# Performance work log

Hardware: AMD Instinct MI355X
Metric: run time of the kernel (lower is better)

Reference implementation:

```python
import jax, jax.numpy as jnp
import numpy as np

HEADS = 8


def setup_inputs() -> dict:
    key = jax.random.key(0)
    ks = jax.random.split(key, 5)
    B, C, H, W = 2, 256, 48, 48
    s = 0.02
    return {
        "ct": jax.random.normal(ks[0], (B, C, H, W), jnp.float32),
        "us": jax.random.normal(ks[1], (B, C, H, W), jnp.float32),
        "w_qkv_ct": jax.random.normal(ks[2], (3 * C, C), jnp.float32) * s,
        "w_qkv_us": jax.random.normal(ks[3], (3 * C, C), jnp.float32) * s,
        "w_proj": jax.random.normal(ks[4], (C, 2 * C), jnp.float32) * s,
        "b_proj": jnp.zeros((C,), jnp.float32),
    }


def _heads_view(x, B, H, W):
    # [B, C, H, W] -> [B, heads, HW, dh]
    C = x.shape[1]
    return x.reshape(B, HEADS, C // HEADS, H * W).transpose(0, 1, 3, 2)


def _cross_attn(q, k, v, scale):
    # q,k,v: [B, heads, HW, dh]
    attn = jax.nn.softmax(jnp.einsum("bhnd,bhmd->bhnm", q, k) * scale, axis=-1)
    return jnp.einsum("bhnm,bhmd->bhnd", attn, v)


def reference(ct, us, w_qkv_ct, w_qkv_us, w_proj, b_proj):
    B, C, H, W = ct.shape
    dh = C // HEADS
    scale = dh ** (-0.5)

    # 1x1 convs as channel GEMMs
    qkv1 = jnp.einsum("oc,bchw->bohw", w_qkv_ct, ct)
    qkv2 = jnp.einsum("oc,bchw->bohw", w_qkv_us, us)
    q1, k1, v1 = jnp.split(qkv1, 3, axis=1)
    q2, k2, v2 = jnp.split(qkv2, 3, axis=1)

    # CT queries attend to US keys/values
    o1 = _cross_attn(_heads_view(q1, B, H, W), _heads_view(k2, B, H, W),
                     _heads_view(v2, B, H, W), scale)
    # US queries attend to CT keys/values
    o2 = _cross_attn(_heads_view(q2, B, H, W), _heads_view(k1, B, H, W),
                     _heads_view(v1, B, H, W), scale)

    # [B, heads, HW, dh] -> [B, C, H, W]
    out1 = o1.transpose(0, 1, 3, 2).reshape(B, C, H, W)
    out2 = o2.transpose(0, 1, 3, 2).reshape(B, C, H, W)

    fused = jnp.concatenate([ct + out1, us + out2], axis=1)
    return jnp.einsum("oc,bchw->bohw", w_proj, fused) + b_proj[None, :, None, None]
```

## Files before the change

### kernel.cpp

```cpp
#include <hip/hip_runtime.h>
#include <hip/hip_bf16.h>
#include <math.h>

#define HW   2304
#define CCH  256

#define QSCALE 0.25504368686637270f

typedef short short8 __attribute__((ext_vector_type(8)));
typedef float f32x4  __attribute__((ext_vector_type(4)));

__device__ inline unsigned short f2bf(float f) {
    union { float f; unsigned u; } v; v.f = f;
    unsigned r = v.u + 0x7FFF + ((v.u >> 16) & 1);
    return (unsigned short)(r >> 16);
}
__device__ inline unsigned pkbf2(float a, float b) {
    float2 f; f.x = a; f.y = b;
    union { __hip_bfloat162 h; unsigned u; } c;
    c.h = __float22bfloat162_rn(f);
    return c.u;
}

__global__ __launch_bounds__(256, 4) void prep_k(
    const float* __restrict__ ct, const float* __restrict__ us,
    const float* __restrict__ w1, const float* __restrict__ w2,
    const float* __restrict__ w3,
    unsigned short* __restrict__ xT,
    unsigned short* __restrict__ b1, unsigned short* __restrict__ b2,
    unsigned short* __restrict__ b3)
{
    const int bx = blockIdx.x, t = threadIdx.x;
    if (bx >= 576) {
        const int u = bx - 576;
        int z, base;
        if (u < 192)      { z = 0; base = u * 1024; }
        else if (u < 384) { z = 1; base = (u - 192) * 1024; }
        else              { z = 2; base = (u - 384) * 1024; }
        const float* s = (z == 0) ? w1 : (z == 1) ? w2 : w3;
        unsigned short* d = (z == 0) ? b1 : (z == 1) ? b2 : b3;
        const int i = base + t * 4;
        const float4 v = *(const float4*)&s[i];
        const float sc = (z < 2 && i < 65536) ? QSCALE : 1.f;
        uint2 p; p.x = pkbf2(v.x * sc, v.y * sc); p.y = pkbf2(v.z * sc, v.w * sc);
        *(uint2*)&d[i] = p;
        return;
    }
    const int u = bx, pt = u % 36, rest = u / 36, ctile = rest & 3, z = rest >> 2;
    const float* __restrict__ src = ((z >> 1) ? us : ct) + (size_t)(z & 1) * CCH * HW;
    unsigned short* __restrict__ dst = xT + (size_t)z * HW * 256;
    const int p0 = pt * 64, c0 = ctile * 64;
    __shared__ __align__(16) unsigned short Ts[64 * 72];
#pragma unroll
    for (int r = 0; r < 4; r++) {
        const int c = (t >> 4) + 16 * r;
        const float4 v = *(const float4*)&src[(size_t)(c0 + c) * HW + p0 + (t & 15) * 4];
        Ts[((t & 15) * 4 + 0) * 72 + c] = f2bf(v.x);
        Ts[((t & 15) * 4 + 1) * 72 + c] = f2bf(v.y);
        Ts[((t & 15) * 4 + 2) * 72 + c] = f2bf(v.z);
        Ts[((t & 15) * 4 + 3) * 72 + c] = f2bf(v.w);
    }
    __syncthreads();
    const int p = t >> 2, c8 = (t & 3) * 16;
    const short8 a  = *(const short8*)&Ts[p * 72 + c8];
    const short8 b8 = *(const short8*)&Ts[p * 72 + c8 + 8];
    *(short8*)&dst[(size_t)(p0 + p) * 256 + c0 + c8]     = a;
    *(short8*)&dst[(size_t)(p0 + p) * 256 + c0 + c8 + 8] = b8;
}

__global__ __launch_bounds__(256, 4) void qkv_k(
    const unsigned short* __restrict__ xT,
    const unsigned short* __restrict__ wb1, const unsigned short* __restrict__ wb2,
    unsigned short* __restrict__ qkvT1, unsigned short* __restrict__ qkvT2,
    unsigned short* __restrict__ vdm1,  unsigned short* __restrict__ vdm2)
{
    const int inp = blockIdx.z >> 1, b = blockIdx.z & 1;
    const unsigned short* __restrict__ X = xT + (size_t)(inp * 2 + b) * HW * 256;
    const unsigned short* __restrict__ W = inp ? wb2 : wb1;
    unsigned short* __restrict__ qT = (inp ? qkvT2 : qkvT1) + (size_t)b * HW * 512;
    unsigned short* __restrict__ vd = (inp ? vdm2 : vdm1) + (size_t)b * CCH * HW;
    const int p0 = blockIdx.x * 64, o0 = blockIdx.y * 64;

    __shared__ __align__(16) unsigned short Ws[64 * 72];
    __shared__ __align__(16) unsigned short Xs[64 * 72];
    const int t = threadIdx.x, w = t >> 6, lane = t & 63, quad = lane >> 4, m = lane & 15;
    const int sr = t >> 3, sc = t & 7;

    f32x4 acc[4] = {{0,0,0,0},{0,0,0,0},{0,0,0,0},{0,0,0,0}};

    for (int k0 = 0; k0 < 256; k0 += 64) {
        const short8 wv0 = *(const short8*)&W[(size_t)(o0 + sr) * 256 + k0 + sc * 8];
        const short8 wv1 = *(const short8*)&W[(size_t)(o0 + 32 + sr) * 256 + k0 + sc * 8];
        const short8 xv0 = *(const short8*)&X[(size_t)(p0 + sr) * 256 + k0 + sc * 8];
        const short8 xv1 = *(const short8*)&X[(size_t)(p0 + 32 + sr) * 256 + k0 + sc * 8];
        __syncthreads();
        *(short8*)&Ws[sr * 72 + sc * 8] = wv0;
        *(short8*)&Ws[(32 + sr) * 72 + sc * 8] = wv1;
        *(short8*)&Xs[sr * 72 + sc * 8] = xv0;
        *(short8*)&Xs[(32 + sr) * 72 + sc * 8] = xv1;
        __syncthreads();
#pragma unroll
        for (int kc2 = 0; kc2 < 2; kc2++) {
            const short8 af = *(const short8*)&Ws[(w * 16 + m) * 72 + kc2 * 32 + quad * 8];
#pragma unroll
            for (int pg = 0; pg < 4; pg++) {
                const short8 bf = *(const short8*)&Xs[(pg * 16 + m) * 72 + kc2 * 32 + quad * 8];
                acc[pg] = __builtin_amdgcn_mfma_f32_16x16x32_bf16(af, bf, acc[pg], 0, 0, 0);
            }
        }
    }

    if (o0 < 512) {
#pragma unroll
        for (int pg = 0; pg < 4; pg++) {
            const int p = p0 + pg * 16 + m;
            uint2 pk; pk.x = pkbf2(acc[pg][0], acc[pg][1]); pk.y = pkbf2(acc[pg][2], acc[pg][3]);
            *(uint2*)&qT[(size_t)p * 512 + o0 + w * 16 + quad * 4] = pk;
        }
    } else {
#pragma unroll
        for (int pg = 0; pg < 4; pg++)
#pragma unroll
            for (int r = 0; r < 4; r++)
                vd[(size_t)(o0 - 512 + w * 16 + quad * 4 + r) * HW + p0 + pg * 16 + m]
                    = f2bf(acc[pg][r]);
    }
}

#define KS_STR 80
#define VS_STR 136
__global__ __launch_bounds__(256, 5) void attn_k(
    const unsigned short* __restrict__ qkvT1, const unsigned short* __restrict__ qkvT2,
    const unsigned short* __restrict__ vdm1,  const unsigned short* __restrict__ vdm2,
    const float* __restrict__ ct, const float* __restrict__ us,
    unsigned short* __restrict__ fusedT)
{
    const int dir = blockIdx.z, b = blockIdx.y >> 3, h = blockIdx.y & 7;
    const unsigned short* __restrict__ Qt = (dir ? qkvT2 : qkvT1) + (size_t)b * HW * 512;
    const unsigned short* __restrict__ Kt = (dir ? qkvT1 : qkvT2) + (size_t)b * HW * 512
                                            + 256 + h * 32;
    const unsigned short* __restrict__ Vd = (dir ? vdm1 : vdm2) + ((size_t)b * CCH + h * 32) * HW;
    const float* __restrict__ src = (dir ? us : ct) + ((size_t)b * CCH + h * 32) * HW;

    const int t = threadIdx.x, w = t >> 6, lane = t & 63, quad = lane >> 4, m = lane & 15;

    __shared__ __align__(16) unsigned short Ks[128 * KS_STR];
    __shared__ __align__(16) unsigned short Vs[32 * VS_STR];

    const int pq = blockIdx.x * 64 + w * 16 + m;
    const short8 qf = *(const short8*)&Qt[(size_t)pq * 512 + h * 32 + quad * 8];

    f32x4 acc0 = {0,0,0,0}, acc1 = {0,0,0,0}, accl = {0,0,0,0};
    const short ONE = (short)0x3F80;
    const short8 ones = {ONE,ONE,ONE,ONE,ONE,ONE,ONE,ONE};

    const int kj0 = t >> 2, kcs = t & 3;
    const int vr0 = t >> 4, vcs = t & 15;
    const int mu = ((m >> 2) * 8 + (m & 3)) * KS_STR + quad * 8;

    for (int j0 = 0; j0 < HW; j0 += 128) {
        const short8 ka = *(const short8*)&Kt[(size_t)(j0 + kj0) * 512 + kcs * 8];
        const short8 kb = *(const short8*)&Kt[(size_t)(j0 + kj0 + 64) * 512 + kcs * 8];
        const short8 va = *(const short8*)&Vd[(size_t)vr0 * HW + j0 + vcs * 8];
        const short8 vb = *(const short8*)&Vd[(size_t)(vr0 + 16) * HW + j0 + vcs * 8];
        __syncthreads();
        *(short8*)&Ks[kj0 * KS_STR + kcs * 8] = ka;
        *(short8*)&Ks[(kj0 + 64) * KS_STR + kcs * 8] = kb;
        *(short8*)&Vs[vr0 * VS_STR + vcs * 8] = va;
        *(short8*)&Vs[(vr0 + 16) * VS_STR + vcs * 8] = vb;
        __syncthreads();

        unsigned pw[16];
#pragma unroll
        for (int f = 0; f < 8; f++) {
            const short8 kf = *(const short8*)&Ks[mu + ((f >> 1) * 32 + (f & 1) * 4) * KS_STR];
            const f32x4 z = {0,0,0,0};
            const f32x4 S = __builtin_amdgcn_mfma_f32_16x16x32_bf16(kf, qf, z, 0, 0, 0);
            pw[f * 2 + 0] = pkbf2(exp2f(S[0]), exp2f(S[1]));
            pw[f * 2 + 1] = pkbf2(exp2f(S[2]), exp2f(S[3]));
        }

#pragma unroll
        for (int kt = 0; kt < 4; kt++) {
            union { short8 s; unsigned u[4]; } bfr;
            bfr.u[0] = pw[4 * kt + 0]; bfr.u[1] = pw[4 * kt + 1];
            bfr.u[2] = pw[4 * kt + 2]; bfr.u[3] = pw[4 * kt + 3];
            const short8 vf0 = *(const short8*)&Vs[m * VS_STR + kt * 32 + quad * 8];
            const short8 vf1 = *(const short8*)&Vs[(16 + m) * VS_STR + kt * 32 + quad * 8];
            acc0 = __builtin_amdgcn_mfma_f32_16x16x32_bf16(vf0, bfr.s, acc0, 0, 0, 0);
            acc1 = __builtin_amdgcn_mfma_f32_16x16x32_bf16(vf1, bfr.s, acc1, 0, 0, 0);
            accl = __builtin_amdgcn_mfma_f32_16x16x32_bf16(ones, bfr.s, accl, 0, 0, 0);
        }
    }

    const float inv = 1.f / accl[0];

    const int cb = dir * 256 + h * 32;
    unsigned short* __restrict__ fT = fusedT + ((size_t)b * HW + pq) * 512 + cb + quad * 4;
    const int d0 = quad * 4;
    uint2 s0, s1;
    s0.x = pkbf2(acc0[0] * inv + src[(size_t)(d0 + 0) * HW + pq],
                 acc0[1] * inv + src[(size_t)(d0 + 1) * HW + pq]);
    s0.y = pkbf2(acc0[2] * inv + src[(size_t)(d0 + 2) * HW + pq],
                 acc0[3] * inv + src[(size_t)(d0 + 3) * HW + pq]);
    s1.x = pkbf2(acc1[0] * inv + src[(size_t)(16 + d0 + 0) * HW + pq],
                 acc1[1] * inv + src[(size_t)(16 + d0 + 1) * HW + pq]);
    s1.y = pkbf2(acc1[2] * inv + src[(size_t)(16 + d0 + 2) * HW + pq],
                 acc1[3] * inv + src[(size_t)(16 + d0 + 3) * HW + pq]);
    *(uint2*)&fT[0]  = s0;
    *(uint2*)&fT[16] = s1;
}

__global__ __launch_bounds__(256, 4) void proj_k(
    const unsigned short* __restrict__ w3b, const unsigned short* __restrict__ fusedT,
    const float* __restrict__ bias, float* __restrict__ out)
{
    const int p0 = blockIdx.x * 64, o0 = blockIdx.y * 64;
    __shared__ __align__(16) unsigned short Ws[64 * 72];
    __shared__ __align__(16) unsigned short Xs[64 * 72];
    const int t = threadIdx.x, w = t >> 6, lane = t & 63, quad = lane >> 4, m = lane & 15;
    const int sr = t >> 3, sc = t & 7;

    f32x4 acc[4] = {{0,0,0,0},{0,0,0,0},{0,0,0,0},{0,0,0,0}};

    for (int k0 = 0; k0 < 512; k0 += 64) {
        const short8 wv0 = *(const short8*)&w3b[(size_t)(o0 + sr) * 512 + k0 + sc * 8];
        const short8 wv1 = *(const short8*)&w3b[(size_t)(o0 + 32 + sr) * 512 + k0 + sc * 8];
        const short8 xv0 = *(const short8*)&fusedT[(size_t)(p0 + sr) * 512 + k0 + sc * 8];
        const short8 xv1 = *(const short8*)&fusedT[(size_t)(p0 + 32 + sr) * 512 + k0 + sc * 8];
        __syncthreads();
        *(short8*)&Ws[sr * 72 + sc * 8] = wv0;
        *(short8*)&Ws[(32 + sr) * 72 + sc * 8] = wv1;
        *(short8*)&Xs[sr * 72 + sc * 8] = xv0;
        *(short8*)&Xs[(32 + sr) * 72 + sc * 8] = xv1;
        __syncthreads();
#pragma unroll
        for (int kc2 = 0; kc2 < 2; kc2++) {
            const short8 af = *(const short8*)&Ws[(w * 16 + m) * 72 + kc2 * 32 + quad * 8];
#pragma unroll
            for (int pg = 0; pg < 4; pg++) {
                const short8 bf = *(const short8*)&Xs[(pg * 16 + m) * 72 + kc2 * 32 + quad * 8];
                acc[pg] = __builtin_amdgcn_mfma_f32_16x16x32_bf16(af, bf, acc[pg], 0, 0, 0);
            }
        }
    }

    const int b = (p0 >= HW) ? 1 : 0;
    const int pl0 = p0 - b * HW;
    float* __restrict__ ob = out + (size_t)b * CCH * HW;
    float b4[4];
#pragma unroll
    for (int r = 0; r < 4; r++) b4[r] = bias[o0 + w * 16 + quad * 4 + r];
#pragma unroll
    for (int pg = 0; pg < 4; pg++)
#pragma unroll
        for (int r = 0; r < 4; r++)
            ob[(size_t)(o0 + w * 16 + quad * 4 + r) * HW + pl0 + pg * 16 + m]
                = acc[pg][r] + b4[r];
}

extern "C" void kernel_launch(void* const* d_in, const int* in_sizes, int n_in,
                              void* d_out, int out_size, void* d_ws, size_t ws_size,
                              hipStream_t stream)
{
    const float* ct       = (const float*)d_in[0];
    const float* us       = (const float*)d_in[1];
    const float* w_qkv_ct = (const float*)d_in[2];
    const float* w_qkv_us = (const float*)d_in[3];
    const float* w_proj   = (const float*)d_in[4];
    const float* b_proj   = (const float*)d_in[5];
    float* out = (float*)d_out;

    unsigned short* wb1   = (unsigned short*)d_ws;
    unsigned short* wb2   = wb1 + (size_t)768 * 256;
    unsigned short* w3b   = wb2 + (size_t)768 * 256;
    unsigned short* xT    = w3b + (size_t)256 * 512;
    unsigned short* qkvT1 = xT    + (size_t)4 * HW * 256;
    unsigned short* qkvT2 = qkvT1 + (size_t)2 * HW * 512;
    unsigned short* vdm1  = qkvT2 + (size_t)2 * HW * 512;
    unsigned short* vdm2  = vdm1  + (size_t)2 * CCH * HW;
    unsigned short* fusedT= vdm2  + (size_t)2 * CCH * HW;

    prep_k<<<dim3(1088), 256, 0, stream>>>(ct, us, w_qkv_ct, w_qkv_us, w_proj,
                                           xT, wb1, wb2, w3b);
    qkv_k <<<dim3(36, 12, 4), 256, 0, stream>>>(xT, wb1, wb2, qkvT1, qkvT2, vdm1, vdm2);
    attn_k<<<dim3(36, 16, 2), 256, 0, stream>>>(qkvT1, qkvT2, vdm1, vdm2, ct, us, fusedT);
    proj_k<<<dim3(72, 4), 256, 0, stream>>>(w3b, fusedT, b_proj, out);
}
```

Measured before the change: 153.2 us.

## Process two query tiles per attention wave and stage QKV epilogue stores through LDS

Each attention wave now handles 32 queries instead of 16, so every K/V tile loaded into shared memory is reused for twice as many queries, and the grid is halved to 18 blocks in x. This cuts K/V global traffic and LDS staging per query, at the cost of more registers (occupancy hint lowered from 5 to 4) and fewer blocks (576) to spread over the GPU. Separately, the QKV projection epilogue writes its results into shared memory first and then issues coalesced 16-byte global stores, replacing scattered 8-byte and 2-byte writes.

```diff
diff --git a/kernel.cpp b/kernel.cpp
--- a/kernel.cpp
+++ b/kernel.cpp
@@ -46,7 +46,7 @@
         *(uint2*)&d[i] = p;
         return;
     }
-    const int u = bx, pt = u % 36, rest = u / 36, ctile = rest & 3, z = rest >> 2;
+    const int pt = bx % 36, rest = bx / 36, ctile = rest & 3, z = rest >> 2;
     const float* __restrict__ src = ((z >> 1) ? us : ct) + (size_t)(z & 1) * CCH * HW;
     unsigned short* __restrict__ dst = xT + (size_t)z * HW * 256;
     const int p0 = pt * 64, c0 = ctile * 64;
@@ -110,26 +110,37 @@
         }
     }
 
+    __syncthreads();
     if (o0 < 512) {
 #pragma unroll
         for (int pg = 0; pg < 4; pg++) {
-            const int p = p0 + pg * 16 + m;
             uint2 pk; pk.x = pkbf2(acc[pg][0], acc[pg][1]); pk.y = pkbf2(acc[pg][2], acc[pg][3]);
-            *(uint2*)&qT[(size_t)p * 512 + o0 + w * 16 + quad * 4] = pk;
-        }
+            *(uint2*)&Ws[(pg * 16 + m) * 72 + w * 16 + quad * 4] = pk;
+        }
+        __syncthreads();
+        const int pr = t >> 2, cc = t & 3;
+        const uint4 d0 = *(const uint4*)&Ws[pr * 72 + cc * 16];
+        const uint4 d1 = *(const uint4*)&Ws[pr * 72 + cc * 16 + 8];
+        *(uint4*)&qT[(size_t)(p0 + pr) * 512 + o0 + cc * 16]     = d0;
+        *(uint4*)&qT[(size_t)(p0 + pr) * 512 + o0 + cc * 16 + 8] = d1;
     } else {
 #pragma unroll
         for (int pg = 0; pg < 4; pg++)
 #pragma unroll
             for (int r = 0; r < 4; r++)
-                vd[(size_t)(o0 - 512 + w * 16 + quad * 4 + r) * HW + p0 + pg * 16 + m]
-                    = f2bf(acc[pg][r]);
+                Ws[(w * 16 + quad * 4 + r) * 72 + pg * 16 + m] = f2bf(acc[pg][r]);
+        __syncthreads();
+        const int dr = t >> 2, cc = t & 3;
+        const uint4 d0 = *(const uint4*)&Ws[dr * 72 + cc * 16];
+        const uint4 d1 = *(const uint4*)&Ws[dr * 72 + cc * 16 + 8];
+        *(uint4*)&vd[(size_t)(o0 - 512 + dr) * HW + p0 + cc * 16]     = d0;
+        *(uint4*)&vd[(size_t)(o0 - 512 + dr) * HW + p0 + cc * 16 + 8] = d1;
     }
 }
 
 #define KS_STR 80
 #define VS_STR 136
-__global__ __launch_bounds__(256, 5) void attn_k(
+__global__ __launch_bounds__(256, 4) void attn_k(
     const unsigned short* __restrict__ qkvT1, const unsigned short* __restrict__ qkvT2,
     const unsigned short* __restrict__ vdm1,  const unsigned short* __restrict__ vdm2,
     const float* __restrict__ ct, const float* __restrict__ us,
@@ -147,10 +158,14 @@
     __shared__ __align__(16) unsigned short Ks[128 * KS_STR];
     __shared__ __align__(16) unsigned short Vs[32 * VS_STR];
 
-    const int pq = blockIdx.x * 64 + w * 16 + m;
-    const short8 qf = *(const short8*)&Qt[(size_t)pq * 512 + h * 32 + quad * 8];
-
-    f32x4 acc0 = {0,0,0,0}, acc1 = {0,0,0,0}, accl = {0,0,0,0};
+    const int pq0 = blockIdx.x * 128 + w * 32 + m;
+    const int pq1 = pq0 + 16;
+    const short8 qf0 = *(const short8*)&Qt[(size_t)pq0 * 512 + h * 32 + quad * 8];
+    const short8 qf1 = *(const short8*)&Qt[(size_t)pq1 * 512 + h * 32 + quad * 8];
+
+    f32x4 acc00 = {0,0,0,0}, acc10 = {0,0,0,0};
+    f32x4 acc01 = {0,0,0,0}, acc11 = {0,0,0,0};
+    f32x4 accl0 = {0,0,0,0}, accl1 = {0,0,0,0};
     const short ONE = (short)0x3F80;
     const short8 ones = {ONE,ONE,ONE,ONE,ONE,ONE,ONE,ONE};
 
@@ -170,45 +185,60 @@
         *(short8*)&Vs[(vr0 + 16) * VS_STR + vcs * 8] = vb;
         __syncthreads();
 
-        unsigned pw[16];
+        unsigned pw0[16], pw1[16];
 #pragma unroll
         for (int f = 0; f < 8; f++) {
             const short8 kf = *(const short8*)&Ks[mu + ((f >> 1) * 32 + (f & 1) * 4) * KS_STR];
             const f32x4 z = {0,0,0,0};
-            const f32x4 S = __builtin_amdgcn_mfma_f32_16x16x32_bf16(kf, qf, z, 0, 0, 0);
-            pw[f * 2 + 0] = pkbf2(exp2f(S[0]), exp2f(S[1]));
-            pw[f * 2 + 1] = pkbf2(exp2f(S[2]), exp2f(S[3]));
+            const f32x4 S0 = __builtin_amdgcn_mfma_f32_16x16x32_bf16(kf, qf0, z, 0, 0, 0);
+            const f32x4 S1 = __builtin_amdgcn_mfma_f32_16x16x32_bf16(kf, qf1, z, 0, 0, 0);
+            pw0[f * 2 + 0] = pkbf2(exp2f(S0[0]), exp2f(S0[1]));
+            pw0[f * 2 + 1] = pkbf2(exp2f(S0[2]), exp2f(S0[3]));
+            pw1[f * 2 + 0] = pkbf2(exp2f(S1[0]), exp2f(S1[1]));
+            pw1[f * 2 + 1] = pkbf2(exp2f(S1[2]), exp2f(S1[3]));
         }
 
 #pragma unroll
         for (int kt = 0; kt < 4; kt++) {
-            union { short8 s; unsigned u[4]; } bfr;
-            bfr.u[0] = pw[4 * kt + 0]; bfr.u[1] = pw[4 * kt + 1];
-            bfr.u[2] = pw[4 * kt + 2]; bfr.u[3] = pw[4 * kt + 3];
+            union { short8 s; unsigned u[4]; } p0u, p1u;
+            p0u.u[0] = pw0[4 * kt + 0]; p0u.u[1] = pw0[4 * kt + 1];
+            p0u.u[2] = pw0[4 * kt + 2]; p0u.u[3] = pw0[4 * kt + 3];
+            p1u.u[0] = pw1[4 * kt + 0]; p1u.u[1] = pw1[4 * kt + 1];
+            p1u.u[2] = pw1[4 * kt + 2]; p1u.u[3] = pw1[4 * kt + 3];
             const short8 vf0 = *(const short8*)&Vs[m * VS_STR + kt * 32 + quad * 8];
             const short8 vf1 = *(const short8*)&Vs[(16 + m) * VS_STR + kt * 32 + quad * 8];
-            acc0 = __builtin_amdgcn_mfma_f32_16x16x32_bf16(vf0, bfr.s, acc0, 0, 0, 0);
-            acc1 = __builtin_amdgcn_mfma_f32_16x16x32_bf16(vf1, bfr.s, acc1, 0, 0, 0);
-            accl = __builtin_amdgcn_mfma_f32_16x16x32_bf16(ones, bfr.s, accl, 0, 0, 0);
-        }
-    }
-
-    const float inv = 1.f / accl[0];
-
-    const int cb = dir * 256 + h * 32;
-    unsigned short* __restrict__ fT = fusedT + ((size_t)b * HW + pq) * 512 + cb + quad * 4;
-    const int d0 = quad * 4;
-    uint2 s0, s1;
-    s0.x = pkbf2(acc0[0] * inv + src[(size_t)(d0 + 0) * HW + pq],
-                 acc0[1] * inv + src[(size_t)(d0 + 1) * HW + pq]);
-    s0.y = pkbf2(acc0[2] * inv + src[(size_t)(d0 + 2) * HW + pq],
-                 acc0[3] * inv + src[(size_t)(d0 + 3) * HW + pq]);
-    s1.x = pkbf2(acc1[0] * inv + src[(size_t)(16 + d0 + 0) * HW + pq],
-                 acc1[1] * inv + src[(size_t)(16 + d0 + 1) * HW + pq]);
-    s1.y = pkbf2(acc1[2] * inv + src[(size_t)(16 + d0 + 2) * HW + pq],
-                 acc1[3] * inv + src[(size_t)(16 + d0 + 3) * HW + pq]);
-    *(uint2*)&fT[0]  = s0;
-    *(uint2*)&fT[16] = s1;
+            acc00 = __builtin_amdgcn_mfma_f32_16x16x32_bf16(vf0, p0u.s, acc00, 0, 0, 0);
+            acc10 = __builtin_amdgcn_mfma_f32_16x16x32_bf16(vf1, p0u.s, acc10, 0, 0, 0);
+            acc01 = __builtin_amdgcn_mfma_f32_16x16x32_bf16(vf0, p1u.s, acc01, 0, 0, 0);
+            acc11 = __builtin_amdgcn_mfma_f32_16x16x32_bf16(vf1, p1u.s, acc11, 0, 0, 0);
+            accl0 = __builtin_amdgcn_mfma_f32_16x16x32_bf16(ones, p0u.s, accl0, 0, 0, 0);
+            accl1 = __builtin_amdgcn_mfma_f32_16x16x32_bf16(ones, p1u.s, accl1, 0, 0, 0);
+        }
+    }
+
+    const float inv0 = 1.f / accl0[0];
+    const float inv1 = 1.f / accl1[0];
+
+    const int cb = dir * 256 + h * 32, d0 = quad * 4;
+#pragma unroll
+    for (int qi = 0; qi < 2; qi++) {
+        const int pq = qi ? pq1 : pq0;
+        const float inv = qi ? inv1 : inv0;
+        const f32x4 aL = qi ? acc01 : acc00;
+        const f32x4 aH = qi ? acc11 : acc10;
+        unsigned short* __restrict__ fT = fusedT + ((size_t)b * HW + pq) * 512 + cb + d0;
+        uint2 s0, s1;
+        s0.x = pkbf2(aL[0] * inv + src[(size_t)(d0 + 0) * HW + pq],
+                     aL[1] * inv + src[(size_t)(d0 + 1) * HW + pq]);
+        s0.y = pkbf2(aL[2] * inv + src[(size_t)(d0 + 2) * HW + pq],
+                     aL[3] * inv + src[(size_t)(d0 + 3) * HW + pq]);
+        s1.x = pkbf2(aH[0] * inv + src[(size_t)(16 + d0 + 0) * HW + pq],
+                     aH[1] * inv + src[(size_t)(16 + d0 + 1) * HW + pq]);
+        s1.y = pkbf2(aH[2] * inv + src[(size_t)(16 + d0 + 2) * HW + pq],
+                     aH[3] * inv + src[(size_t)(16 + d0 + 3) * HW + pq]);
+        *(uint2*)&fT[0]  = s0;
+        *(uint2*)&fT[16] = s1;
+    }
 }
 
 __global__ __launch_bounds__(256, 4) void proj_k(
@@ -284,6 +314,6 @@
     prep_k<<<dim3(1088), 256, 0, stream>>>(ct, us, w_qkv_ct, w_qkv_us, w_proj,
                                            xT, wb1, wb2, w3b);
     qkv_k <<<dim3(36, 12, 4), 256, 0, stream>>>(xT, wb1, wb2, qkvT1, qkvT2, vdm1, vdm2);
-    attn_k<<<dim3(36, 16, 2), 256, 0, stream>>>(qkvT1, qkvT2, vdm1, vdm2, ct, us, fusedT);
+    attn_k<<<dim3(18, 16, 2), 256, 0, stream>>>(qkvT1, qkvT2, vdm1, vdm2, ct, us, fusedT);
     proj_k<<<dim3(72, 4), 256, 0, stream>>>(w3b, fusedT, b_proj, out);
 }
```

After: 163.5 us. +6.7%, slower.
